# Performance work log

Measured on AMD Instinct MI355X. Metric: run time of the kernel, lower is better.

## Reference

```python
import jax, jax.numpy as jnp
import numpy as np

DT = 0.01  # module-level constant in the original source
H = 64


def _lstm_cell(x_in, h, c, W_ih, W_hh, b_ih, b_hh):
    # torch nn.LSTM gate order: i, f, g, o
    gates = x_in @ W_ih.T + h @ W_hh.T + (b_ih + b_hh)
    i, f, g, o = jnp.split(gates, 4, axis=-1)
    i = jax.nn.sigmoid(i)
    f = jax.nn.sigmoid(f)
    g = jnp.tanh(g)
    o = jax.nn.sigmoid(o)
    c_new = f * c + i * g
    h_new = o * jnp.tanh(c_new)
    return h_new, c_new


def setup_inputs() -> dict:
    key = jax.random.key(0)
    ks = jax.random.split(key, 12)
    B, x_size, s_size = 4096, 8, 8
    in_size = x_size + s_size
    sc = 1.0 / np.sqrt(H)

    def rn(k, shape, scale=1.0):
        return (jax.random.normal(k, shape, dtype=jnp.float32) * scale)

    return {
        "x": rn(ks[0], (B, 1, x_size)),
        "s0": rn(ks[1], (B, s_size)),
        "W_ih0": rn(ks[2], (4 * H, in_size), sc),
        "W_hh0": rn(ks[3], (4 * H, H), sc),
        "b_ih0": rn(ks[4], (4 * H,), sc),
        "b_hh0": rn(ks[5], (4 * H,), sc),
        "W_ih1": rn(ks[6], (4 * H, H), sc),
        "W_hh1": rn(ks[7], (4 * H, H), sc),
        "b_ih1": rn(ks[8], (4 * H,), sc),
        "b_hh1": rn(ks[9], (4 * H,), sc),
        "fc_W": rn(ks[10], (s_size, H), sc),
        "fc_b": rn(ks[11], (s_size,), sc),
        "num_steps": 1001,  # floor(max_time/dt)+1 with max_time=10.0
    }


def reference(x, s0, W_ih0, W_hh0, b_ih0, b_hh0, W_ih1, W_hh1, b_ih1, b_hh1,
              fc_W, fc_b, num_steps):
    B = x.shape[0]
    xin = x[:, 0, :]  # forward only ever reads x[:, 0:1] -> [B, x_size]
    h0 = jnp.zeros((B, H), x.dtype)

    def step(carry, _):
        s, h_a, c_a, h_b, c_b = carry
        combined = jnp.concatenate([xin, s], axis=-1)  # [B, x_size + s_size]
        h_a, c_a = _lstm_cell(combined, h_a, c_a, W_ih0, W_hh0, b_ih0, b_hh0)
        h_b, c_b = _lstm_cell(h_a, h_b, c_b, W_ih1, W_hh1, b_ih1, b_hh1)
        step_out = h_b @ fc_W.T + fc_b            # [B, s_size]
        s_new = s + step_out * DT                  # Euler integration
        return (s_new, h_a, c_a, h_b, c_b), (s_new, step_out)

    init = (s0, h0, h0, h0, h0)
    _, (outs, res) = jax.lax.scan(step, init, None, length=num_steps)
    outputs = jnp.transpose(outs, (1, 0, 2))       # [B, num_steps, s_size]
    res_step = jnp.transpose(res, (1, 0, 2))       # [B, num_steps, s_size]
    cal_times = jnp.arange(num_steps, dtype=jnp.float32) * DT
    return outputs, cal_times, res_step
```

## Files before the change

kernel.cpp:

```cpp
#include <hip/hip_runtime.h>

#define DTC 0.01f

typedef __attribute__((ext_vector_type(8))) short short8;
typedef __attribute__((ext_vector_type(4))) float floatx4;

#if __has_builtin(__builtin_amdgcn_exp2f)
#define EXP2F(x) __builtin_amdgcn_exp2f(x)
#else
#define EXP2F(x) exp2f(x)
#endif
#if __has_builtin(__builtin_amdgcn_rcpf)
#define RCPF(x) __builtin_amdgcn_rcpf(x)
#else
#define RCPF(x) (1.0f / (x))
#endif

__device__ __forceinline__ unsigned short f2bf(float f) {
    unsigned u = __float_as_uint(f);
    u += 0x7FFFu + ((u >> 16) & 1u);
    return (unsigned short)(u >> 16);
}
__device__ __forceinline__ float sigm(float x) {
    float e = EXP2F(-1.44269504089f * x);
    return RCPF(1.0f + e);
}
__device__ __forceinline__ float tanh_f(float x) {
    float e = EXP2F(2.88539008178f * x);
    return 1.0f - 2.0f * RCPF(e + 1.0f);
}

#define U0S 104
#define U1S 136

__global__ __launch_bounds__(256, 1) void lstm_mfma(
    const float* __restrict__ x,    const float* __restrict__ s0,
    const float* __restrict__ W_ih0,const float* __restrict__ W_hh0,
    const float* __restrict__ b_ih0,const float* __restrict__ b_hh0,
    const float* __restrict__ W_ih1,const float* __restrict__ W_hh1,
    const float* __restrict__ b_ih1,const float* __restrict__ b_hh1,
    const float* __restrict__ fc_W, const float* __restrict__ fc_b,
    const int* __restrict__ nsp,    float* __restrict__ out, int B)
{
    __shared__ unsigned short U0[16 * U0S];
    __shared__ unsigned short U1[16 * U1S];

    const int ns   = nsp[0];
    const int tid  = threadIdx.x;
    const int lane = tid & 63;
    const int wave = tid >> 6;
    const int il   = lane & 15;
    const int quad = lane >> 4;
    const int bb   = blockIdx.x * 16;

    float* cal = out + (size_t)B * ns * 8;
    float* res = cal + ns;

    if (blockIdx.x == 0)
        for (int t = tid; t < ns; t += 256) cal[t] = t * DTC;

    for (int i = tid; i < 16 * U0S; i += 256) U0[i] = 0;
    for (int i = tid; i < 16 * U1S; i += 256) U1[i] = 0;

    short8 B0[4][3], B1[4][4], BF[2];
    floatx4 bias0[4];
    float bias1[4];
    for (int j = 0; j < 4; ++j) {
        const int n = 64 * j + 16 * wave + il;
        for (int kk = 0; kk < 3; ++kk) {
            short8 f;
            #pragma unroll
            for (int jj = 0; jj < 8; ++jj) {
                int k = 32 * kk + 8 * quad + jj;
                float w;
                if (k < 64)      w = W_hh0[n * 64 + k];
                else if (k < 72) w = W_ih0[n * 16 + 8 + (k - 64)];
                else             w = 0.0f;
                f[jj] = (short)f2bf(w);
            }
            B0[j][kk] = f;
        }
        for (int kk = 0; kk < 4; ++kk) {
            short8 f;
            #pragma unroll
            for (int jj = 0; jj < 8; ++jj) {
                int k = 32 * kk + 8 * quad + jj;
                float w = (k < 64) ? W_ih1[n * 64 + k] : W_hh1[n * 64 + (k - 64)];
                f[jj] = (short)f2bf(w);
            }
            B1[j][kk] = f;
        }
        float bcol = b_ih0[n] + b_hh0[n];
        floatx4 bv;
        #pragma unroll
        for (int reg = 0; reg < 4; ++reg) {
            int m = 4 * quad + reg;
            float acc = bcol;
            for (int k = 0; k < 8; ++k)
                acc += x[(bb + m) * 8 + k] * W_ih0[n * 16 + k];
            bv[reg] = acc;
        }
        bias0[j] = bv;
        bias1[j] = b_ih1[n] + b_hh1[n];
    }
    for (int kk = 0; kk < 2; ++kk) {
        short8 f;
        #pragma unroll
        for (int jj = 0; jj < 8; ++jj) {
            int k = 32 * kk + 8 * quad + jj;
            float w = (il < 8) ? fc_W[il * 64 + k] : 0.0f;
            f[jj] = (short)f2bf(w);
        }
        BF[kk] = f;
    }
    const float fcb = (il < 8) ? fc_b[il] : 0.0f;

    float cA[4] = {0, 0, 0, 0}, cB[4] = {0, 0, 0, 0};
    float s_reg[4];
    #pragma unroll
    for (int reg = 0; reg < 4; ++reg) {
        int m = 4 * quad + reg;
        s_reg[reg] = (il < 8) ? s0[(bb + m) * 8 + il] : 0.0f;
    }
    if (wave == 0 && il < 8) {
        #pragma unroll
        for (int reg = 0; reg < 4; ++reg)
            U0[(4 * quad + reg) * U0S + 64 + il] = f2bf(s_reg[reg]);
    }
    __syncthreads();

    const int iidx = 16 * wave + il;

    #pragma unroll 1
    for (int t = 0; t < ns; ++t) {
        short8 a00 = *(const short8*)&U0[il * U0S + 0  + 8 * quad];
        short8 a01 = *(const short8*)&U0[il * U0S + 32 + 8 * quad];
        short8 a02 = *(const short8*)&U0[il * U0S + 64 + 8 * quad];
        short8 a12 = *(const short8*)&U1[il * U1S + 64 + 8 * quad];
        short8 a13 = *(const short8*)&U1[il * U1S + 96 + 8 * quad];
        __syncthreads();

        floatx4 g0[4];
        #pragma unroll
        for (int j = 0; j < 4; ++j) {
            floatx4 acc = bias0[j];
            acc = __builtin_amdgcn_mfma_f32_16x16x32_bf16(a00, B0[j][0], acc, 0, 0, 0);
            acc = __builtin_amdgcn_mfma_f32_16x16x32_bf16(a01, B0[j][1], acc, 0, 0, 0);
            acc = __builtin_amdgcn_mfma_f32_16x16x32_bf16(a02, B0[j][2], acc, 0, 0, 0);
            g0[j] = acc;
        }
        #pragma unroll
        for (int reg = 0; reg < 4; ++reg) {
            float ig = sigm(g0[0][reg]);
            float fg = sigm(g0[1][reg]);
            float gg = tanh_f(g0[2][reg]);
            float og = sigm(g0[3][reg]);
            float c  = fg * cA[reg] + ig * gg;
            cA[reg]  = c;
            unsigned short hb = f2bf(og * tanh_f(c));
            int m = 4 * quad + reg;
            U0[m * U0S + iidx] = hb;
            U1[m * U1S + iidx] = hb;
        }
        __syncthreads();

        short8 a10 = *(const short8*)&U1[il * U1S + 0  + 8 * quad];
        short8 a11 = *(const short8*)&U1[il * U1S + 32 + 8 * quad];
        floatx4 g1[4];
        #pragma unroll
        for (int j = 0; j < 4; ++j) {
            floatx4 acc = {bias1[j], bias1[j], bias1[j], bias1[j]};
            acc = __builtin_amdgcn_mfma_f32_16x16x32_bf16(a10, B1[j][0], acc, 0, 0, 0);
            acc = __builtin_amdgcn_mfma_f32_16x16x32_bf16(a11, B1[j][1], acc, 0, 0, 0);
            acc = __builtin_amdgcn_mfma_f32_16x16x32_bf16(a12, B1[j][2], acc, 0, 0, 0);
            acc = __builtin_amdgcn_mfma_f32_16x16x32_bf16(a13, B1[j][3], acc, 0, 0, 0);
            g1[j] = acc;
        }
        #pragma unroll
        for (int reg = 0; reg < 4; ++reg) {
            float ig = sigm(g1[0][reg]);
            float fg = sigm(g1[1][reg]);
            float gg = tanh_f(g1[2][reg]);
            float og = sigm(g1[3][reg]);
            float c  = fg * cB[reg] + ig * gg;
            cB[reg]  = c;
            int m = 4 * quad + reg;
            U1[m * U1S + 64 + iidx] = f2bf(og * tanh_f(c));
        }
        __syncthreads();

        short8 af0 = *(const short8*)&U1[il * U1S + 64 + 8 * quad];
        short8 af1 = *(const short8*)&U1[il * U1S + 96 + 8 * quad];
        floatx4 so = {fcb, fcb, fcb, fcb};
        so = __builtin_amdgcn_mfma_f32_16x16x32_bf16(af0, BF[0], so, 0, 0, 0);
        so = __builtin_amdgcn_mfma_f32_16x16x32_bf16(af1, BF[1], so, 0, 0, 0);

        #pragma unroll
        for (int reg = 0; reg < 4; ++reg) s_reg[reg] += so[reg] * DTC;

        if (wave == 0 && il < 8) {
            #pragma unroll
            for (int reg = 0; reg < 4; ++reg) {
                int m = 4 * quad + reg;
                U0[m * U0S + 64 + il] = f2bf(s_reg[reg]);
                size_t o = ((size_t)(bb + m) * ns + t) * 8 + il;
                out[o] = s_reg[reg];
                res[o] = so[reg];
            }
        }
        __syncthreads();
    }
}

extern "C" void kernel_launch(void* const* d_in, const int* in_sizes, int n_in,
                              void* d_out, int out_size, void* d_ws, size_t ws_size,
                              hipStream_t stream) {
    const float* x     = (const float*)d_in[0];
    const float* s0    = (const float*)d_in[1];
    const float* W_ih0 = (const float*)d_in[2];
    const float* W_hh0 = (const float*)d_in[3];
    const float* b_ih0 = (const float*)d_in[4];
    const float* b_hh0 = (const float*)d_in[5];
    const float* W_ih1 = (const float*)d_in[6];
    const float* W_hh1 = (const float*)d_in[7];
    const float* b_ih1 = (const float*)d_in[8];
    const float* b_hh1 = (const float*)d_in[9];
    const float* fc_W  = (const float*)d_in[10];
    const float* fc_b  = (const float*)d_in[11];
    const int*   nsp   = (const int*)d_in[12];
    (void)d_ws; (void)ws_size; (void)n_in; (void)out_size;
    int B = in_sizes[0] / 8;
    dim3 grid(B / 16), block(256);
    hipLaunchKernelGGL(lstm_mfma, grid, block, 0, stream,
        x, s0, W_ih0, W_hh0, b_ih0, b_hh0, W_ih1, W_hh1, b_ih1, b_hh1,
        fc_W, fc_b, nsp, (float*)d_out, B);
}
```

Before: 1.545 ms.

## Remove per-step FC barrier via transposed MFMA and split gate work across 8 waves

The fc projection now uses a transposed MFMA (fc weights as A, h_b as B), so each lane holds the state for its own batch row. The state is packed into the layer-0 input fragment through a lane shuffle instead of going through shared memory, which removes the third barrier in each timestep. The block grows to 512 threads, with two waves per gate column group each handling half of the elementwise rows, and shared-memory tiles shrink. The trade-off is duplicated MFMA work across the wave pairs, larger blocks, and barriers that now span more waves.

```diff
diff --git a/kernel.cpp b/kernel.cpp
--- a/kernel.cpp
+++ b/kernel.cpp
@@ -16,10 +16,10 @@
 #define RCPF(x) (1.0f / (x))
 #endif
 
-__device__ __forceinline__ unsigned short f2bf(float f) {
+__device__ __forceinline__ unsigned f2bf(float f) {
     unsigned u = __float_as_uint(f);
     u += 0x7FFFu + ((u >> 16) & 1u);
-    return (unsigned short)(u >> 16);
+    return u >> 16;
 }
 __device__ __forceinline__ float sigm(float x) {
     float e = EXP2F(-1.44269504089f * x);
@@ -30,10 +30,10 @@
     return 1.0f - 2.0f * RCPF(e + 1.0f);
 }
 
-#define U0S 104
-#define U1S 136
-
-__global__ __launch_bounds__(256, 1) void lstm_mfma(
+#define U0S 72
+#define U1S 72
+
+__global__ __launch_bounds__(512, 2) void lstm_mfma(
     const float* __restrict__ x,    const float* __restrict__ s0,
     const float* __restrict__ W_ih0,const float* __restrict__ W_hh0,
     const float* __restrict__ b_ih0,const float* __restrict__ b_hh0,
@@ -49,6 +49,8 @@
     const int tid  = threadIdx.x;
     const int lane = tid & 63;
     const int wave = tid >> 6;
+    const int wq   = wave & 3;
+    const int r0   = (wave >> 2) * 2;
     const int il   = lane & 15;
     const int quad = lane >> 4;
     const int bb   = blockIdx.x * 16;
@@ -57,16 +59,16 @@
     float* res = cal + ns;
 
     if (blockIdx.x == 0)
-        for (int t = tid; t < ns; t += 256) cal[t] = t * DTC;
-
-    for (int i = tid; i < 16 * U0S; i += 256) U0[i] = 0;
-    for (int i = tid; i < 16 * U1S; i += 256) U1[i] = 0;
-
-    short8 B0[4][3], B1[4][4], BF[2];
+        for (int t = tid; t < ns; t += 512) cal[t] = t * DTC;
+
+    for (int i = tid; i < 16 * U0S; i += 512) U0[i] = 0;
+    for (int i = tid; i < 16 * U1S; i += 512) U1[i] = 0;
+
+    short8 B0[4][3], B1[4][4], FA[2];
     floatx4 bias0[4];
     float bias1[4];
     for (int j = 0; j < 4; ++j) {
-        const int n = 64 * j + 16 * wave + il;
+        const int n = 64 * j + 16 * wq + il;
         for (int kk = 0; kk < 3; ++kk) {
             short8 f;
             #pragma unroll
@@ -111,33 +113,56 @@
             float w = (il < 8) ? fc_W[il * 64 + k] : 0.0f;
             f[jj] = (short)f2bf(w);
         }
-        BF[kk] = f;
+        FA[kk] = f;
     }
-    const float fcb = (il < 8) ? fc_b[il] : 0.0f;
-
-    float cA[4] = {0, 0, 0, 0}, cB[4] = {0, 0, 0, 0};
-    float s_reg[4];
+    floatx4 biasT;
     #pragma unroll
-    for (int reg = 0; reg < 4; ++reg) {
-        int m = 4 * quad + reg;
-        s_reg[reg] = (il < 8) ? s0[(bb + m) * 8 + il] : 0.0f;
-    }
-    if (wave == 0 && il < 8) {
-        #pragma unroll
-        for (int reg = 0; reg < 4; ++reg)
-            U0[(4 * quad + reg) * U0S + 64 + il] = f2bf(s_reg[reg]);
-    }
+    for (int reg = 0; reg < 4; ++reg)
+        biasT[reg] = (quad < 2) ? fc_b[4 * quad + reg] : 0.0f;
+
+    float cA[2] = {0, 0}, cB[2] = {0, 0};
+    floatx4 sT;
+    #pragma unroll
+    for (int reg = 0; reg < 4; ++reg)
+        sT[reg] = (quad < 2) ? s0[(bb + il) * 8 + 4 * quad + reg] : 0.0f;
+    unsigned pk0 = f2bf(sT[0]) | (f2bf(sT[1]) << 16);
+    unsigned pk1 = f2bf(sT[2]) | (f2bf(sT[3]) << 16);
     __syncthreads();
 
-    const int iidx = 16 * wave + il;
+    const int iidx = 16 * wq + il;
 
     #pragma unroll 1
-    for (int t = 0; t < ns; ++t) {
+    for (int t = 0; ; ++t) {
         short8 a00 = *(const short8*)&U0[il * U0S + 0  + 8 * quad];
         short8 a01 = *(const short8*)&U0[il * U0S + 32 + 8 * quad];
-        short8 a02 = *(const short8*)&U0[il * U0S + 64 + 8 * quad];
-        short8 a12 = *(const short8*)&U1[il * U1S + 64 + 8 * quad];
-        short8 a13 = *(const short8*)&U1[il * U1S + 96 + 8 * quad];
+        short8 a12 = *(const short8*)&U1[il * U1S + 0  + 8 * quad];
+        short8 a13 = *(const short8*)&U1[il * U1S + 32 + 8 * quad];
+
+        if (t > 0) {
+            floatx4 so = biasT;
+            so = __builtin_amdgcn_mfma_f32_16x16x32_bf16(FA[1], a13, so, 0, 0, 0);
+            so = __builtin_amdgcn_mfma_f32_16x16x32_bf16(FA[0], a12, so, 0, 0, 0);
+            #pragma unroll
+            for (int reg = 0; reg < 4; ++reg) sT[reg] += so[reg] * DTC;
+            pk0 = f2bf(sT[0]) | (f2bf(sT[1]) << 16);
+            pk1 = f2bf(sT[2]) | (f2bf(sT[3]) << 16);
+            if (wave == 0 && quad < 2) {
+                size_t o = ((size_t)(bb + il) * ns + (t - 1)) * 8 + 4 * quad;
+                *(floatx4*)(out + o) = sT;
+                *(floatx4*)(res + o) = so;
+            }
+        }
+        if (t == ns) break;
+
+        int sh0 = __shfl((int)pk0, (lane + 16) & 63, 64);
+        int sh1 = __shfl((int)pk1, (lane + 16) & 63, 64);
+        union { int i[4]; short8 s8; } ua;
+        ua.i[0] = (quad == 0) ? (int)pk0 : 0;
+        ua.i[1] = (quad == 0) ? (int)pk1 : 0;
+        ua.i[2] = (quad == 0) ? sh0 : 0;
+        ua.i[3] = (quad == 0) ? sh1 : 0;
+        short8 a02 = ua.s8;
+
         __syncthreads();
 
         floatx4 g0[4];
@@ -150,22 +175,20 @@
             g0[j] = acc;
         }
         #pragma unroll
-        for (int reg = 0; reg < 4; ++reg) {
+        for (int rr = 0; rr < 2; ++rr) {
+            int reg = r0 + rr;
             float ig = sigm(g0[0][reg]);
             float fg = sigm(g0[1][reg]);
             float gg = tanh_f(g0[2][reg]);
             float og = sigm(g0[3][reg]);
-            float c  = fg * cA[reg] + ig * gg;
-            cA[reg]  = c;
-            unsigned short hb = f2bf(og * tanh_f(c));
-            int m = 4 * quad + reg;
-            U0[m * U0S + iidx] = hb;
-            U1[m * U1S + iidx] = hb;
+            float c  = fg * cA[rr] + ig * gg;
+            cA[rr]   = c;
+            U0[(4 * quad + reg) * U0S + iidx] = (unsigned short)f2bf(og * tanh_f(c));
         }
         __syncthreads();
 
-        short8 a10 = *(const short8*)&U1[il * U1S + 0  + 8 * quad];
-        short8 a11 = *(const short8*)&U1[il * U1S + 32 + 8 * quad];
+        short8 a10 = *(const short8*)&U0[il * U0S + 0  + 8 * quad];
+        short8 a11 = *(const short8*)&U0[il * U0S + 32 + 8 * quad];
         floatx4 g1[4];
         #pragma unroll
         for (int j = 0; j < 4; ++j) {
@@ -177,36 +200,15 @@
             g1[j] = acc;
         }
         #pragma unroll
-        for (int reg = 0; reg < 4; ++reg) {
+        for (int rr = 0; rr < 2; ++rr) {
+            int reg = r0 + rr;
             float ig = sigm(g1[0][reg]);
             float fg = sigm(g1[1][reg]);
             float gg = tanh_f(g1[2][reg]);
             float og = sigm(g1[3][reg]);
-            float c  = fg * cB[reg] + ig * gg;
-            cB[reg]  = c;
-            int m = 4 * quad + reg;
-            U1[m * U1S + 64 + iidx] = f2bf(og * tanh_f(c));
-        }
-        __syncthreads();
-
-        short8 af0 = *(const short8*)&U1[il * U1S + 64 + 8 * quad];
-        short8 af1 = *(const short8*)&U1[il * U1S + 96 + 8 * quad];
-        floatx4 so = {fcb, fcb, fcb, fcb};
-        so = __builtin_amdgcn_mfma_f32_16x16x32_bf16(af0, BF[0], so, 0, 0, 0);
-        so = __builtin_amdgcn_mfma_f32_16x16x32_bf16(af1, BF[1], so, 0, 0, 0);
-
-        #pragma unroll
-        for (int reg = 0; reg < 4; ++reg) s_reg[reg] += so[reg] * DTC;
-
-        if (wave == 0 && il < 8) {
-            #pragma unroll
-            for (int reg = 0; reg < 4; ++reg) {
-                int m = 4 * quad + reg;
-                U0[m * U0S + 64 + il] = f2bf(s_reg[reg]);
-                size_t o = ((size_t)(bb + m) * ns + t) * 8 + il;
-                out[o] = s_reg[reg];
-                res[o] = so[reg];
-            }
+            float c  = fg * cB[rr] + ig * gg;
+            cB[rr]   = c;
+            U1[(4 * quad + reg) * U1S + iidx] = (unsigned short)f2bf(og * tanh_f(c));
         }
         __syncthreads();
     }
@@ -230,7 +232,7 @@
     const int*   nsp   = (const int*)d_in[12];
     (void)d_ws; (void)ws_size; (void)n_in; (void)out_size;
     int B = in_sizes[0] / 8;
-    dim3 grid(B / 16), block(256);
+    dim3 grid(B / 16), block(512);
     hipLaunchKernelGGL(lstm_mfma, grid, block, 0, stream,
         x, s0, W_ih0, W_hh0, b_ih0, b_hh0, W_ih1, W_hh1, b_ih1, b_hh1,
         fc_W, fc_b, nsp, (float*)d_out, B);
```

After: 1.622 ms. +5.0%, slower.
